# Kernel optimization log

Measured on AMD Instinct MI355X. Metric: run time of the kernel, lower is better.

## Reference

```python
import jax, jax.numpy as jnp
import numpy as np

DIM = 256          # inter_dim
GROUPS = 32        # GroupNorm groups
P = 8              # patch_size (square)
EPS = 1e-5


def group_norm(x, gamma, beta):
    # x: (b, c, h, w); normalize over (c/G, h, w) per group, biased variance (torch default)
    b, c, h, w = x.shape
    xg = x.reshape(b, GROUPS, -1)
    m = xg.mean(-1, keepdims=True)
    v = xg.var(-1, keepdims=True)
    xn = ((xg - m) * jax.lax.rsqrt(v + EPS)).reshape(b, c, h, w)
    return xn * gamma[None, :, None, None] + beta[None, :, None, None]


def to_patches(x):
    # 'b c (h p1) (w p2) -> (b h w) c (p1 p2)'
    b, c, H, W = x.shape
    nh, nw = H // P, W // P
    x = x.reshape(b, c, nh, P, nw, P).transpose(0, 2, 4, 1, 3, 5)  # b nh nw c p1 p2
    return x.reshape(b * nh * nw, c, P * P)


def from_patches(x, b, H, W):
    # '(b h w) c (p1 p2) -> b c (h p1) (w p2)'
    nh, nw = H // P, W // P
    c = x.shape[1]
    x = x.reshape(b, nh, nw, c, P, P).transpose(0, 3, 1, 4, 2, 5)
    return x.reshape(b, c, H, W)


def setup_inputs() -> dict:
    key = jax.random.key(0)
    ks = jax.random.split(key, 4)
    b, c, H, W = 8, 256, 128, 128
    return {
        "x_low": jax.random.normal(ks[0], (b, c, H, W), jnp.float32),
        "x_high": jax.random.normal(ks[1], (b, c, H, W), jnp.float32),
        "wq": jax.random.normal(ks[2], (DIM, c), jnp.float32) * (1.0 / np.sqrt(c)),
        "wk": jax.random.normal(ks[3], (DIM, c), jnp.float32) * (1.0 / np.sqrt(c)),
        "gq": jnp.ones((DIM,), jnp.float32),
        "bq": jnp.zeros((DIM,), jnp.float32),
        "gk": jnp.ones((DIM,), jnp.float32),
        "bk": jnp.zeros((DIM,), jnp.float32),
    }


def reference(x_low, x_high, wq, wk, gq, bq, gk, bk):
    b, c, H, W = x_low.shape
    # 1x1 conv (bias-free) + GroupNorm for q and k projections
    q = group_norm(jnp.einsum('oc,bchw->bohw', wq, x_low), gq, bq)
    k = group_norm(jnp.einsum('oc,bchw->bohw', wk, x_high), gk, bk)
    qp = to_patches(q).transpose(0, 2, 1)   # (n_windows, p, c)
    kp = to_patches(k)                      # (n_windows, c, p)
    attn = jax.nn.softmax(jnp.matmul(qp, kp) / jnp.sqrt(jnp.float32(DIM)), axis=-1)  # (n, p, p)
    out = jnp.matmul(attn, kp.transpose(0, 2, 1))  # (n, p, c)
    out = from_patches(out.transpose(0, 2, 1), b, H, W)
    return out + x_low
```

## Files before the change

kernel.cpp:

```cpp
#include <hip/hip_runtime.h>
#include <hip/hip_bf16.h>

using short8  = __attribute__((ext_vector_type(8))) short;
using short4v = __attribute__((ext_vector_type(4))) short;
using fx4     = __attribute__((ext_vector_type(4))) float;
using fx2     = __attribute__((ext_vector_type(2))) float;

#define NB 8
#define CDIM 256
#define HH 128
#define NPIX 16384
#define NG_ELEMS 131072.0f

#define XS_STRIDE 66

__device__ __forceinline__ float bf2f(short s) {
    union { unsigned u; float f; } c; c.u = ((unsigned)(unsigned short)s) << 16; return c.f;
}
__device__ __forceinline__ short f2bf(float f) {
    union { float f; unsigned u; } c; c.f = f;
    unsigned u = c.u;
    u += 0x7FFFu + ((u >> 16) & 1u);
    return (short)(u >> 16);
}
__device__ __forceinline__ short2 f2bf2(float a, float b) {
    __hip_bfloat162 h = __float22bfloat162_rn(make_float2(a, b));
    union { __hip_bfloat162 b; short2 s; } c; c.b = h; return c.s;
}

__global__ __launch_bounds__(256) void kW(const float* __restrict__ wq,
                                          const float* __restrict__ wk,
                                          short* __restrict__ WB) {
    int kc = blockIdx.x;
    int t  = blockIdx.y;
    const float* W = t ? wk : wq;
    int tid = threadIdx.x;
    int ntile = tid >> 4, lr = tid & 15;
    int n = ntile * 16 + lr;
#pragma unroll
    for (int quad = 0; quad < 4; ++quad) {
        const float* p = W + (size_t)n * CDIM + kc * 32 + quad * 8;
        fx4 v0 = *(const fx4*)p;
        fx4 v1 = *(const fx4*)(p + 4);
        union { short8 v; short2 h[4]; } s;
        s.h[0] = f2bf2(v0[0], v0[1]);
        s.h[1] = f2bf2(v0[2], v0[3]);
        s.h[2] = f2bf2(v1[0], v1[1]);
        s.h[3] = f2bf2(v1[2], v1[3]);
        *(short8*)(WB + ((((size_t)t * 8 + kc) * 16 + ntile) * 64 + quad * 16 + lr) * 8) = s.v;
    }
}

__global__ __launch_bounds__(256, 2) void kG(const float* __restrict__ xlo,
                                             const float* __restrict__ xhi,
                                             const short* __restrict__ WB,
                                             short* __restrict__ qt,
                                             short* __restrict__ kt,
                                             fx2* __restrict__ partials) {
    __shared__ float Xs[256 * XS_STRIDE];

    int m0 = blockIdx.x * 64;
    int zy = blockIdx.y;
    int b = zy >> 1, t = zy & 1;
    const float* X = (t ? xhi : xlo) + (size_t)b * CDIM * NPIX;
    const short* WBt = WB + (size_t)t * 8 * 16 * 64 * 8;
    short* OUT = (t ? kt : qt) + (size_t)b * NPIX * CDIM;
    int tid = threadIdx.x;
    int w = tid >> 6, l = tid & 63, lr = l & 15, quad = l >> 4;

    {
        int cbase = w * 64;
#pragma unroll
        for (int cc = 0; cc < 64; ++cc) {
            int c = cbase + cc;
            __builtin_amdgcn_global_load_lds(
                (const __attribute__((address_space(1))) void*)(X + (size_t)c * NPIX + m0 + l),
                (__attribute__((address_space(3))) void*)(&Xs[c * XS_STRIDE]),
                4, 0, 0);
        }
    }
    __syncthreads();

    fx4 acc[4][4];
#pragma unroll
    for (int m = 0; m < 4; ++m)
#pragma unroll
        for (int n = 0; n < 4; ++n) { acc[m][n][0]=0.f; acc[m][n][1]=0.f; acc[m][n][2]=0.f; acc[m][n][3]=0.f; }

#pragma unroll
    for (int kc = 0; kc < 8; ++kc) {
        short8 af[4];
        const short* wb = WBt + (((size_t)kc * 16 + w * 4) * 64 + l) * 8;
#pragma unroll
        for (int m = 0; m < 4; ++m)
            af[m] = *(const short8*)(wb + (size_t)m * 64 * 8);

        const float* xq = &Xs[(kc * 32 + quad * 8) * XS_STRIDE + lr];
#pragma unroll
        for (int nt = 0; nt < 4; ++nt) {
            union { short8 v; short2 h[4]; } s;
#pragma unroll
            for (int j = 0; j < 4; ++j) {
                float a = xq[(2 * j    ) * XS_STRIDE + nt * 16];
                float bv = xq[(2 * j + 1) * XS_STRIDE + nt * 16];
                s.h[j] = f2bf2(a, bv);
            }
            short8 bf = s.v;
#pragma unroll
            for (int m = 0; m < 4; ++m)
                acc[m][nt] = __builtin_amdgcn_mfma_f32_16x16x32_bf16(af[m], bf, acc[m][nt], 0, 0, 0);
        }
    }

    {
        float gs[4], gss[4];
#pragma unroll
        for (int m = 0; m < 4; ++m) {
            gs[m] = 0.f; gss[m] = 0.f;
#pragma unroll
            for (int r = 0; r < 4; ++r) {
                float a0 = acc[m][0][r], a1 = acc[m][1][r], a2 = acc[m][2][r], a3 = acc[m][3][r];
                float sv = (a0 + a1) + (a2 + a3);
                float sq = (a0 * a0 + a1 * a1) + (a2 * a2 + a3 * a3);
                sv += __shfl_xor(sv, 1);  sq += __shfl_xor(sq, 1);
                sv += __shfl_xor(sv, 2);  sq += __shfl_xor(sq, 2);
                sv += __shfl_xor(sv, 4);  sq += __shfl_xor(sq, 4);
                sv += __shfl_xor(sv, 8);  sq += __shfl_xor(sq, 8);
                sv += __shfl_xor(sv, 16); sq += __shfl_xor(sq, 16);
                gs[m] += sv; gss[m] += sq;
            }
        }
        if (l == 0 || l == 32) {
            int h = l >> 5;
            fx2* pp = partials + ((size_t)zy * 256 + blockIdx.x) * 32 + w * 8 + h;
#pragma unroll
            for (int m = 0; m < 4; ++m) {
                fx2 v; v[0] = gs[m]; v[1] = gss[m];
                pp[m * 2] = v;
            }
        }
    }

#pragma unroll
    for (int n = 0; n < 4; ++n) {
        int pix = m0 + n * 16 + lr;
        short* op = OUT + (size_t)pix * CDIM + w * 64 + quad * 4;
#pragma unroll
        for (int m = 0; m < 4; ++m) {
            short2 p0 = f2bf2(acc[m][n][0], acc[m][n][1]);
            short2 p1 = f2bf2(acc[m][n][2], acc[m][n][3]);
            short4v v; v[0] = p0.x; v[1] = p0.y; v[2] = p1.x; v[3] = p1.y;
            *(short4v*)(op + m * 16) = v;
        }
    }
}

__global__ __launch_bounds__(256) void kR(const fx2* __restrict__ partials,
                                          float* __restrict__ stats) {
    __shared__ fx2 red[8][32];
    int zy = blockIdx.x;
    int b = zy >> 1, t = zy & 1;
    int tid = threadIdx.x;
    int j = tid >> 5, slot = tid & 31;
    fx2 acc; acc[0] = 0.f; acc[1] = 0.f;
#pragma unroll
    for (int i = 0; i < 32; ++i) {
        fx2 v = partials[((size_t)zy * 256 + j * 32 + i) * 32 + slot];
        acc[0] += v[0]; acc[1] += v[1];
    }
    red[j][slot] = acc;
    __syncthreads();
    if (tid < 32) {
        fx2 s = red[0][tid];
#pragma unroll
        for (int jj = 1; jj < 8; ++jj) { s[0] += red[jj][tid][0]; s[1] += red[jj][tid][1]; }
        float* st = stats + ((size_t)(t * NB + b) * 32 + tid) * 2;
        st[0] = s[0];
        st[1] = s[1];
    }
}

__global__ __launch_bounds__(256) void kS(const float* __restrict__ stats,
                                          const float* __restrict__ gq,
                                          const float* __restrict__ bq,
                                          const float* __restrict__ gk,
                                          const float* __restrict__ bk,
                                          float* __restrict__ scale,
                                          float* __restrict__ shift) {
    int id = blockIdx.x * 256 + threadIdx.x;
    int t = id >> 11, b = (id >> 8) & 7, o = id & 255;
    int g = o >> 3;
    const float* st = stats + ((size_t)(t * NB + b) * 32 + g) * 2;
    float mean = st[0] * (1.0f / NG_ELEMS);
    float var  = st[1] * (1.0f / NG_ELEMS) - mean * mean;
    float rstd = rsqrtf(var + 1e-5f);
    float gamma = (t ? gk : gq)[o];
    float beta  = (t ? bk : bq)[o];
    float sc = gamma * rstd;
    scale[id] = sc;
    shift[id] = beta - mean * sc;
}

__global__ __launch_bounds__(256) void kA(const short* __restrict__ qt,
                                          const short* __restrict__ kt,
                                          const float* __restrict__ scale,
                                          const float* __restrict__ shift,
                                          const float* __restrict__ xlo,
                                          float* __restrict__ outp) {
    __shared__ short Ks[64 * 264];
    __shared__ float SsF[64 * 68];
    __shared__ short Ps[64 * 72];
    short* Os = (short*)SsF;

    int blk = blockIdx.x;
    int b = blk >> 8, wh = (blk >> 4) & 15, ww = blk & 15;
    int tid = threadIdx.x;
    int w = tid >> 6, l = tid & 63, lr = l & 15, quad = l >> 4;

    const float* sq = scale + (size_t)b * CDIM;
    const float* zq = shift + (size_t)b * CDIM;
    const float* sk = scale + (size_t)(NB + b) * CDIM;
    const float* zk = shift + (size_t)(NB + b) * CDIM;

    {
        int oct = tid & 31;
        int j00 = tid >> 5;
        float skv[8], zkv[8];
#pragma unroll
        for (int e = 0; e < 8; ++e) { skv[e] = sk[oct * 8 + e]; zkv[e] = zk[oct * 8 + e]; }
#pragma unroll
        for (int it = 0; it < 8; ++it) {
            int j = j00 + it * 8;
            int pix = (wh * 8 + (j >> 3)) * HH + ww * 8 + (j & 7);
            short8 kv = *(const short8*)(kt + ((size_t)b * NPIX + pix) * CDIM + oct * 8);
            short8 nv;
#pragma unroll
            for (int e = 0; e < 8; ++e) nv[e] = f2bf(bf2f(kv[e]) * skv[e] + zkv[e]);
            *(short8*)(&Ks[j * 264 + oct * 8]) = nv;
        }
    }
    __syncthreads();

    {
        fx4 accS[4];
#pragma unroll
        for (int nt = 0; nt < 4; ++nt) { accS[nt][0]=0.f; accS[nt][1]=0.f; accS[nt][2]=0.f; accS[nt][3]=0.f; }
        int qi = 16 * w + lr;
        int pixq = (wh * 8 + (qi >> 3)) * HH + ww * 8 + (qi & 7);
        const short* qrow = qt + ((size_t)b * NPIX + pixq) * CDIM;
#pragma unroll
        for (int kc = 0; kc < 8; ++kc) {
            int c0 = kc * 32 + quad * 8;
            short8 qv = *(const short8*)(qrow + c0);
            short8 aq;
#pragma unroll
            for (int e = 0; e < 8; ++e) aq[e] = f2bf(bf2f(qv[e]) * sq[c0 + e] + zq[c0 + e]);
#pragma unroll
            for (int nt = 0; nt < 4; ++nt) {
                short8 bk8 = *(const short8*)(&Ks[(nt * 16 + lr) * 264 + c0]);
                accS[nt] = __builtin_amdgcn_mfma_f32_16x16x32_bf16(aq, bk8, accS[nt], 0, 0, 0);
            }
        }
#pragma unroll
        for (int nt = 0; nt < 4; ++nt)
#pragma unroll
            for (int r = 0; r < 4; ++r)
                SsF[(16 * w + quad * 4 + r) * 68 + nt * 16 + lr] = accS[nt][r] * 0.0625f;
    }
    __syncthreads();

    {
        int row = tid >> 2, seg = tid & 3;
        float v[16];
#pragma unroll
        for (int k4 = 0; k4 < 4; ++k4) {
            fx4 t4 = *(const fx4*)(&SsF[row * 68 + seg * 16 + k4 * 4]);
            v[k4*4+0] = t4[0]; v[k4*4+1] = t4[1]; v[k4*4+2] = t4[2]; v[k4*4+3] = t4[3];
        }
        float m = v[0];
#pragma unroll
        for (int e = 1; e < 16; ++e) m = fmaxf(m, v[e]);
        m = fmaxf(m, __shfl_xor(m, 1));
        m = fmaxf(m, __shfl_xor(m, 2));
        float s = 0.f;
#pragma unroll
        for (int e = 0; e < 16; ++e) { v[e] = __expf(v[e] - m); s += v[e]; }
        s += __shfl_xor(s, 1);
        s += __shfl_xor(s, 2);
        float inv = 1.0f / s;
        short8 p0, p1;
#pragma unroll
        for (int e = 0; e < 8; ++e) { p0[e] = f2bf(v[e] * inv); p1[e] = f2bf(v[8 + e] * inv); }
        *(short8*)(&Ps[row * 72 + seg * 16]) = p0;
        *(short8*)(&Ps[row * 72 + seg * 16 + 8]) = p1;
    }
    __syncthreads();

    fx4 accO[4][4];
#pragma unroll
    for (int mt = 0; mt < 4; ++mt)
#pragma unroll
        for (int nt = 0; nt < 4; ++nt) { accO[mt][nt][0]=0.f; accO[mt][nt][1]=0.f; accO[mt][nt][2]=0.f; accO[mt][nt][3]=0.f; }
#pragma unroll
    for (int kc2 = 0; kc2 < 2; ++kc2) {
        int j0 = kc2 * 32 + quad * 8;
        short8 ap[4];
#pragma unroll
        for (int mt = 0; mt < 4; ++mt)
            ap[mt] = *(const short8*)(&Ps[(mt * 16 + lr) * 72 + j0]);
#pragma unroll
        for (int nt = 0; nt < 4; ++nt) {
            int c = 64 * w + nt * 16 + lr;
            short8 bk8;
#pragma unroll
            for (int jj = 0; jj < 8; ++jj) bk8[jj] = Ks[(j0 + jj) * 264 + c];
#pragma unroll
            for (int mt = 0; mt < 4; ++mt)
                accO[mt][nt] = __builtin_amdgcn_mfma_f32_16x16x32_bf16(ap[mt], bk8, accO[mt][nt], 0, 0, 0);
        }
    }

    int half = w >> 1;
#pragma unroll
    for (int h2 = 0; h2 < 2; ++h2) {
        __syncthreads();
        if (half == h2) {
#pragma unroll
            for (int mt = 0; mt < 4; ++mt)
#pragma unroll
                for (int nt = 0; nt < 4; ++nt) {
                    int i = mt * 16 + quad * 4;
                    int cl = 64 * w + nt * 16 + lr - 128 * h2;
#pragma unroll
                    for (int r = 0; r < 4; ++r)
                        Os[(i + r) * 136 + cl] = f2bf(accO[mt][nt][r]);
                }
        }
        __syncthreads();
#pragma unroll
        for (int it = 0; it < 4; ++it) {
            int id = tid + it * 256;
            int cl = id & 127, h = id >> 7;
            int cg = cl + 128 * h2;
            size_t gidx = ((size_t)(b * CDIM + cg)) * NPIX + (size_t)(wh * 8 + h) * HH + ww * 8;
            fx4 x0 = *(const fx4*)(xlo + gidx);
            fx4 x1 = *(const fx4*)(xlo + gidx + 4);
            fx4 r0, r1;
#pragma unroll
            for (int jj = 0; jj < 4; ++jj) {
                r0[jj] = bf2f(Os[(h * 8 + jj)     * 136 + cl]) + x0[jj];
                r1[jj] = bf2f(Os[(h * 8 + 4 + jj) * 136 + cl]) + x1[jj];
            }
            *(fx4*)(outp + gidx)     = r0;
            *(fx4*)(outp + gidx + 4) = r1;
        }
    }
}

extern "C" void kernel_launch(void* const* d_in, const int* in_sizes, int n_in,
                              void* d_out, int out_size, void* d_ws, size_t ws_size,
                              hipStream_t stream) {
    const float* xlo = (const float*)d_in[0];
    const float* xhi = (const float*)d_in[1];
    const float* wqp = (const float*)d_in[2];
    const float* wkp = (const float*)d_in[3];
    const float* gq  = (const float*)d_in[4];
    const float* bq  = (const float*)d_in[5];
    const float* gk  = (const float*)d_in[6];
    const float* bk  = (const float*)d_in[7];
    float* outp = (float*)d_out;
    char* ws = (char*)d_ws;
    size_t SZB = (size_t)NB * NPIX * CDIM * 2;
    short* qt    = (short*)(ws);
    short* kt    = (short*)(ws + SZB);
    float* stats = (float*)(ws + 2 * SZB);
    float* scale = (float*)(ws + 2 * SZB + 4096);
    float* shift = (float*)(ws + 2 * SZB + 4096 + 16384);
    short* WB    = (short*)(ws + 2 * SZB + 4096 + 32768);
    fx2*   partials = (fx2*)(ws + 2 * SZB + 4096 + 32768 + 262144);

    kW<<<dim3(8, 2), dim3(256), 0, stream>>>(wqp, wkp, WB);
    kG<<<dim3(256, 16), dim3(256), 0, stream>>>(xlo, xhi, WB, qt, kt, partials);
    kR<<<dim3(16), dim3(256), 0, stream>>>(partials, stats);
    kS<<<dim3(16), dim3(256), 0, stream>>>(stats, gq, bq, gk, bk, scale, shift);
    kA<<<dim3(2048), dim3(256), 0, stream>>>(qt, kt, scale, shift, xlo, outp);
}
```

Before: 560.1 us.

## Do softmax in registers, alias output staging onto K tile, remap block order

Softmax now runs directly on the MFMA accumulators using cross-lane shuffles, so the fp32 score tile in shared memory and one barrier are gone. The output staging buffer reuses the K tile's shared memory, which lets the whole 64x256 output be written in one pass instead of two halves with extra barriers. Dropping the score buffer shrinks shared memory use, and a launch bound of 3 blocks per CU is requested to raise occupancy. Block indices are also remapped so consecutive blocks handle different batches. The tighter register budget may cause spills, and the scattered 2-byte writes to the probability tile may add bank conflicts.

```diff
diff --git a/kernel.cpp b/kernel.cpp
--- a/kernel.cpp
+++ b/kernel.cpp
@@ -201,18 +201,18 @@
     shift[id] = beta - mean * sc;
 }
 
-__global__ __launch_bounds__(256) void kA(const short* __restrict__ qt,
-                                          const short* __restrict__ kt,
-                                          const float* __restrict__ scale,
-                                          const float* __restrict__ shift,
-                                          const float* __restrict__ xlo,
-                                          float* __restrict__ outp) {
+__global__ __launch_bounds__(256, 3) void kA(const short* __restrict__ qt,
+                                             const short* __restrict__ kt,
+                                             const float* __restrict__ scale,
+                                             const float* __restrict__ shift,
+                                             const float* __restrict__ xlo,
+                                             float* __restrict__ outp) {
     __shared__ short Ks[64 * 264];
-    __shared__ float SsF[64 * 68];
     __shared__ short Ps[64 * 72];
-    short* Os = (short*)SsF;
-
-    int blk = blockIdx.x;
+    short* Os = &Ks[0];
+
+    int bid = blockIdx.x;
+    int blk = ((bid & 7) << 8) | (bid >> 3);
     int b = blk >> 8, wh = (blk >> 4) & 15, ww = blk & 15;
     int tid = threadIdx.x;
     int w = tid >> 6, l = tid & 63, lr = l & 15, quad = l >> 4;
@@ -262,37 +262,28 @@
             }
         }
 #pragma unroll
-        for (int nt = 0; nt < 4; ++nt)
-#pragma unroll
-            for (int r = 0; r < 4; ++r)
-                SsF[(16 * w + quad * 4 + r) * 68 + nt * 16 + lr] = accS[nt][r] * 0.0625f;
-    }
-    __syncthreads();
-
-    {
-        int row = tid >> 2, seg = tid & 3;
-        float v[16];
-#pragma unroll
-        for (int k4 = 0; k4 < 4; ++k4) {
-            fx4 t4 = *(const fx4*)(&SsF[row * 68 + seg * 16 + k4 * 4]);
-            v[k4*4+0] = t4[0]; v[k4*4+1] = t4[1]; v[k4*4+2] = t4[2]; v[k4*4+3] = t4[3];
-        }
-        float m = v[0];
-#pragma unroll
-        for (int e = 1; e < 16; ++e) m = fmaxf(m, v[e]);
-        m = fmaxf(m, __shfl_xor(m, 1));
-        m = fmaxf(m, __shfl_xor(m, 2));
-        float s = 0.f;
-#pragma unroll
-        for (int e = 0; e < 16; ++e) { v[e] = __expf(v[e] - m); s += v[e]; }
-        s += __shfl_xor(s, 1);
-        s += __shfl_xor(s, 2);
-        float inv = 1.0f / s;
-        short8 p0, p1;
-#pragma unroll
-        for (int e = 0; e < 8; ++e) { p0[e] = f2bf(v[e] * inv); p1[e] = f2bf(v[8 + e] * inv); }
-        *(short8*)(&Ps[row * 72 + seg * 16]) = p0;
-        *(short8*)(&Ps[row * 72 + seg * 16 + 8]) = p1;
+        for (int r = 0; r < 4; ++r) {
+            float v0 = accS[0][r] * 0.0625f, v1 = accS[1][r] * 0.0625f;
+            float v2 = accS[2][r] * 0.0625f, v3 = accS[3][r] * 0.0625f;
+            float m = fmaxf(fmaxf(v0, v1), fmaxf(v2, v3));
+            m = fmaxf(m, __shfl_xor(m, 1));
+            m = fmaxf(m, __shfl_xor(m, 2));
+            m = fmaxf(m, __shfl_xor(m, 4));
+            m = fmaxf(m, __shfl_xor(m, 8));
+            float p0 = __expf(v0 - m), p1 = __expf(v1 - m);
+            float p2 = __expf(v2 - m), p3 = __expf(v3 - m);
+            float s = (p0 + p1) + (p2 + p3);
+            s += __shfl_xor(s, 1);
+            s += __shfl_xor(s, 2);
+            s += __shfl_xor(s, 4);
+            s += __shfl_xor(s, 8);
+            float inv = 1.0f / s;
+            int row = 16 * w + quad * 4 + r;
+            Ps[row * 72 +  0 + lr] = f2bf(p0 * inv);
+            Ps[row * 72 + 16 + lr] = f2bf(p1 * inv);
+            Ps[row * 72 + 32 + lr] = f2bf(p2 * inv);
+            Ps[row * 72 + 48 + lr] = f2bf(p3 * inv);
+        }
     }
     __syncthreads();
 
@@ -320,39 +311,35 @@
         }
     }
 
-    int half = w >> 1;
-#pragma unroll
-    for (int h2 = 0; h2 < 2; ++h2) {
-        __syncthreads();
-        if (half == h2) {
-#pragma unroll
-            for (int mt = 0; mt < 4; ++mt)
-#pragma unroll
-                for (int nt = 0; nt < 4; ++nt) {
-                    int i = mt * 16 + quad * 4;
-                    int cl = 64 * w + nt * 16 + lr - 128 * h2;
-#pragma unroll
-                    for (int r = 0; r < 4; ++r)
-                        Os[(i + r) * 136 + cl] = f2bf(accO[mt][nt][r]);
-                }
-        }
-        __syncthreads();
-#pragma unroll
-        for (int it = 0; it < 4; ++it) {
-            int id = tid + it * 256;
-            int cl = id & 127, h = id >> 7;
-            int cg = cl + 128 * h2;
-            size_t gidx = ((size_t)(b * CDIM + cg)) * NPIX + (size_t)(wh * 8 + h) * HH + ww * 8;
-            fx4 x0 = *(const fx4*)(xlo + gidx);
-            fx4 x1 = *(const fx4*)(xlo + gidx + 4);
+    __syncthreads();
+#pragma unroll
+    for (int mt = 0; mt < 4; ++mt)
+#pragma unroll
+        for (int nt = 0; nt < 4; ++nt) {
+            int i = mt * 16 + quad * 4;
+            int c = 64 * w + nt * 16 + lr;
+#pragma unroll
+            for (int r = 0; r < 4; ++r)
+                Os[(i + r) * 264 + c] = f2bf(accO[mt][nt][r]);
+        }
+    __syncthreads();
+
+    {
+        int cl = tid;
+        const float* xrow = xlo + ((size_t)(b * CDIM + cl)) * NPIX + (size_t)(wh * 8) * HH + ww * 8;
+        float* orow = outp + ((size_t)(b * CDIM + cl)) * NPIX + (size_t)(wh * 8) * HH + ww * 8;
+#pragma unroll
+        for (int h = 0; h < 8; ++h) {
+            fx4 x0 = *(const fx4*)(xrow + (size_t)h * HH);
+            fx4 x1 = *(const fx4*)(xrow + (size_t)h * HH + 4);
             fx4 r0, r1;
 #pragma unroll
             for (int jj = 0; jj < 4; ++jj) {
-                r0[jj] = bf2f(Os[(h * 8 + jj)     * 136 + cl]) + x0[jj];
-                r1[jj] = bf2f(Os[(h * 8 + 4 + jj) * 136 + cl]) + x1[jj];
-            }
-            *(fx4*)(outp + gidx)     = r0;
-            *(fx4*)(outp + gidx + 4) = r1;
+                r0[jj] = bf2f(Os[(h * 8 + jj)     * 264 + cl]) + x0[jj];
+                r1[jj] = bf2f(Os[(h * 8 + 4 + jj) * 264 + cl]) + x1[jj];
+            }
+            *(fx4*)(orow + (size_t)h * HH)     = r0;
+            *(fx4*)(orow + (size_t)h * HH + 4) = r1;
         }
     }
 }
```

Result: faster. 500.5 us (-10.6%).
